# Kernel optimization log

Hardware: AMD Instinct MI355X
Metric: run time of the kernel (lower is better)

Reference implementation:

```python
import jax, jax.numpy as jnp
import numpy as np

B, L, D, H = 2, 4096, 1024, 1  # head_dim == embed_dim in source, forcing H=1


def setup_inputs() -> dict:
    key = jax.random.key(0)
    k_x, kq, kk, kv, ko = jax.random.split(key, 5)
    s = 1.0 / np.sqrt(D)
    return {
        "x": jax.random.normal(k_x, (B, L, D), dtype=jnp.float32),
        "W_q": jax.random.normal(kq, (D, D), dtype=jnp.float32) * s,
        "W_k": jax.random.normal(kk, (D, D), dtype=jnp.float32) * s,
        "W_v": jax.random.normal(kv, (D, D), dtype=jnp.float32) * s,
        "W_o": jax.random.normal(ko, (D, D), dtype=jnp.float32) * s,
    }


def reference(x, W_q, W_k, W_v, W_o):
    # nn.Linear(y) = y @ W.T ; weights stored as (out, in)
    Hd = D  # head_dim = embed_dim (source quirk), so num_heads must be 1
    Q = jnp.einsum('bld,ed->ble', x, W_q).reshape(B, L, H, Hd).transpose(0, 2, 1, 3)
    K = jnp.einsum('bld,ed->ble', x, W_k).reshape(B, L, H, Hd).transpose(0, 2, 1, 3)
    V = jnp.einsum('bld,ed->ble', x, W_v).reshape(B, L, H, Hd).transpose(0, 2, 1, 3)
    scores = jnp.einsum('bhqd,bhkd->bhqk', Q, K) / jnp.sqrt(jnp.float32(Hd))
    attn = jax.nn.softmax(scores, axis=-1)
    out = jnp.einsum('bhqk,bhkd->bhqd', attn, V)  # (B,H,L,Hd)
    out = out.transpose(0, 2, 1, 3).reshape(B, L, D)
    return jnp.einsum('bld,ed->ble', out, W_o)
```

## Files before the change

### kernel.cpp

```cpp
#include <hip/hip_runtime.h>
#include <hip/hip_bf16.h>
#include <stdint.h>


typedef unsigned short u16;
typedef short short8 __attribute__((ext_vector_type(8)));
typedef float f32x4 __attribute__((ext_vector_type(4)));

__device__ __forceinline__ void async_ld16(void* lds, const void* g) {
  __builtin_amdgcn_global_load_lds(
      (const __attribute__((address_space(1))) unsigned int*)g,
      (__attribute__((address_space(3))) unsigned int*)lds,
      16, 0, 0);
}

__device__ __forceinline__ u16 f2bf(float f) {
  unsigned u = __float_as_uint(f);
  u += 0x7FFFu + ((u >> 16) & 1u);
  return (u16)(u >> 16);
}

__global__ __launch_bounds__(256)
void cast_f32_bf16(const float* __restrict__ in, u16* __restrict__ out, int n) {
  const int i = (blockIdx.x * 256 + threadIdx.x) * 8;
  if (i >= n) return;
  float4 a = ((const float4*)(in + i))[0];
  float4 b = ((const float4*)(in + i))[1];
  uint4 o;
  o.x = (unsigned)f2bf(a.x) | ((unsigned)f2bf(a.y) << 16);
  o.y = (unsigned)f2bf(a.z) | ((unsigned)f2bf(a.w) << 16);
  o.z = (unsigned)f2bf(b.x) | ((unsigned)f2bf(b.y) << 16);
  o.w = (unsigned)f2bf(b.z) | ((unsigned)f2bf(b.w) << 16);
  *(uint4*)(out + i) = o;
}

__global__ __launch_bounds__(256)
void cast_w4_bf16(const float* __restrict__ w0, const float* __restrict__ w1,
                  const float* __restrict__ w2, const float* __restrict__ w3,
                  u16* __restrict__ out) {
  const int idx = (blockIdx.x * 256 + threadIdx.x) * 8;
  const int which = idx >> 20;
  const int off = idx & 1048575;
  const float* src = which == 0 ? w0 : which == 1 ? w1 : which == 2 ? w2 : w3;
  float4 a = ((const float4*)(src + off))[0];
  float4 b = ((const float4*)(src + off))[1];
  uint4 o;
  o.x = (unsigned)f2bf(a.x) | ((unsigned)f2bf(a.y) << 16);
  o.y = (unsigned)f2bf(a.z) | ((unsigned)f2bf(a.w) << 16);
  o.z = (unsigned)f2bf(b.x) | ((unsigned)f2bf(b.y) << 16);
  o.w = (unsigned)f2bf(b.z) | ((unsigned)f2bf(b.w) << 16);
  *(uint4*)(out + idx) = o;
}

#define BM 128
#define BN 128
#define BK 32

template <int XSWZ>
__global__ __launch_bounds__(256)
void gemm_bt(const u16* __restrict__ A, const u16* __restrict__ Bt,
             void* __restrict__ Cv, int K, int lda, int ldb, int ldc,
             long long sAz, long long sBz, long long sCz,
             float scale, int store_f32) {
  __shared__ u16 As[3][BM * BK];
  __shared__ u16 Bs[3][BN * BK];

  int bx, by, bz;
  if constexpr (XSWZ) {
    const int gx = gridDim.x, gy = gridDim.y;
    const int nwg = gx * gy * gridDim.z;
    const int lin = (blockIdx.z * gy + blockIdx.y) * gx + blockIdx.x;
    const int chunk = nwg >> 3;
    const int swz = (lin & 7) * chunk + (lin >> 3);
    bx = swz % gx;
    const int t1 = swz / gx;
    by = t1 % gy;
    bz = t1 / gy;
  } else {
    bx = blockIdx.x; by = blockIdx.y; bz = blockIdx.z;
  }

  A  += (long long)bz * sAz;
  Bt += (long long)bz * sBz;

  const int tid  = threadIdx.x;
  const int wave = tid >> 6;
  const int lane = tid & 63;
  const int wm   = wave >> 1;
  const int wn   = wave & 1;
  const int r15  = lane & 15;
  const int q4   = lane >> 4;

  const int tileM = by * BM;
  const int tileN = bx * BN;

  const int srow = tid >> 2;
  const int scol = ((tid & 3) ^ (srow & 3)) * 8;

  const u16* Aptr = A + (long long)tileM * lda + scol;
  const u16* Bptr = Bt + (long long)tileN * ldb + scol;

  auto stage = [&](int kt) {
    const int b = kt % 3;
    const int k0 = kt * BK;
    u16* as = &As[b][tid * 8];
    u16* bs = &Bs[b][tid * 8];
    async_ld16(as,        Aptr + (long long)srow * lda + k0);
    async_ld16(as + 2048, Aptr + (long long)(srow + 64) * lda + k0);
    async_ld16(bs,        Bptr + (long long)srow * ldb + k0);
    async_ld16(bs + 2048, Bptr + (long long)(srow + 64) * ldb + k0);
  };

  f32x4 zero = {0.f, 0.f, 0.f, 0.f};
  f32x4 acc[4][4];
#pragma unroll
  for (int i = 0; i < 4; ++i)
#pragma unroll
    for (int j = 0; j < 4; ++j) acc[i][j] = zero;

  const int csw = ((q4 ^ (r15 & 3)) * 8);

  const int NT = K / BK;
  stage(0);
  if (NT > 1) stage(1);
  if (NT > 2) stage(2);

  for (int kt = 0; kt < NT; ++kt) {
    const int rem = NT - 1 - kt;
    if (rem >= 2)      asm volatile("s_waitcnt vmcnt(8)" ::: "memory");
    else if (rem == 1) asm volatile("s_waitcnt vmcnt(4)" ::: "memory");
    else               asm volatile("s_waitcnt vmcnt(0)" ::: "memory");
    __builtin_amdgcn_s_barrier();

    const int b = kt % 3;
    const u16* as = &As[b][0];
    const u16* bs = &Bs[b][0];

    short8 af[4], bf[4];
#pragma unroll
    for (int i = 0; i < 4; ++i)
      af[i] = *(const short8*)&as[(wm * 64 + i * 16 + r15) * BK + csw];
#pragma unroll
    for (int i = 0; i < 4; ++i)
      bf[i] = *(const short8*)&bs[(wn * 64 + i * 16 + r15) * BK + csw];

    __builtin_amdgcn_s_setprio(1);
#pragma unroll
    for (int i = 0; i < 4; ++i)
#pragma unroll
      for (int j = 0; j < 4; ++j)
        acc[i][j] = __builtin_amdgcn_mfma_f32_16x16x32_bf16(af[i], bf[j], acc[i][j], 0, 0, 0);
    __builtin_amdgcn_s_setprio(0);

    __builtin_amdgcn_s_barrier();
    if (kt + 3 < NT) stage(kt + 3);
  }

#pragma unroll
  for (int i = 0; i < 4; ++i) {
#pragma unroll
    for (int j = 0; j < 4; ++j) {
      const int col = tileN + wn * 64 + j * 16 + r15;
#pragma unroll
      for (int r = 0; r < 4; ++r) {
        const int row = tileM + wm * 64 + i * 16 + q4 * 4 + r;
        const long long idx = (long long)bz * sCz + (long long)row * ldc + col;
        const float val = acc[i][j][r] * scale;
        if (store_f32) ((float*)Cv)[idx] = val;
        else           ((u16*)Cv)[idx] = f2bf(val);
      }
    }
  }
}

__global__ __launch_bounds__(256)
void softmax_rows(u16* __restrict__ S) {
  const int tid = threadIdx.x;
  u16* rp = S + (long long)blockIdx.x * 4096;

  uint4 a = ((const uint4*)rp)[tid * 2];
  uint4 b = ((const uint4*)rp)[tid * 2 + 1];
  unsigned w[8] = {a.x, a.y, a.z, a.w, b.x, b.y, b.z, b.w};
  float v[16];
#pragma unroll
  for (int i = 0; i < 8; ++i) {
    v[2 * i]     = __uint_as_float(w[i] << 16);
    v[2 * i + 1] = __uint_as_float(w[i] & 0xFFFF0000u);
  }

  float m = v[0];
#pragma unroll
  for (int i = 1; i < 16; ++i) m = fmaxf(m, v[i]);
#pragma unroll
  for (int o = 32; o > 0; o >>= 1) m = fmaxf(m, __shfl_xor(m, o));
  __shared__ float redm[4];
  __shared__ float reds[4];
  const int wave = tid >> 6;
  if ((tid & 63) == 0) redm[wave] = m;
  __syncthreads();
  m = fmaxf(fmaxf(redm[0], redm[1]), fmaxf(redm[2], redm[3]));

  float s = 0.f;
#pragma unroll
  for (int i = 0; i < 16; ++i) {
    v[i] = __expf(v[i] - m);
    s += v[i];
  }
#pragma unroll
  for (int o = 32; o > 0; o >>= 1) s += __shfl_xor(s, o);
  if ((tid & 63) == 0) reds[wave] = s;
  __syncthreads();
  s = (reds[0] + reds[1]) + (reds[2] + reds[3]);
  const float inv = 1.0f / s;

#pragma unroll
  for (int i = 0; i < 8; ++i)
    w[i] = (unsigned)f2bf(v[2 * i] * inv) | ((unsigned)f2bf(v[2 * i + 1] * inv) << 16);
  uint4 oa = {w[0], w[1], w[2], w[3]};
  uint4 ob = {w[4], w[5], w[6], w[7]};
  ((uint4*)rp)[tid * 2] = oa;
  ((uint4*)rp)[tid * 2 + 1] = ob;
}

extern "C" void kernel_launch(void* const* d_in, const int* in_sizes, int n_in,
                              void* d_out, int out_size, void* d_ws, size_t ws_size,
                              hipStream_t stream) {
  const float* x  = (const float*)d_in[0];
  const float* Wq = (const float*)d_in[1];
  const float* Wk = (const float*)d_in[2];
  const float* Wv = (const float*)d_in[3];
  const float* Wo = (const float*)d_in[4];
  float* out = (float*)d_out;

  u16* xb  = (u16*)d_ws;
  u16* Wqb = xb  + 8388608;
  u16* Wkb = Wqb + 1048576;
  u16* Wvb = Wkb + 1048576;
  u16* Wob = Wvb + 1048576;
  u16* QKp = Wob + 1048576;
  u16* Vt  = QKp + 16777216;
  u16* S   = Vt  + 8388608;
  u16* O   = QKp;

  const dim3 blk(256);

  cast_f32_bf16<<<dim3(4096), blk, 0, stream>>>(x, xb, 8388608);
  cast_w4_bf16<<<dim3(2048), blk, 0, stream>>>(Wq, Wk, Wv, Wo, Wqb);

  gemm_bt<1><<<dim3(16, 64, 1), blk, 0, stream>>>(xb, Wqb, QKp,
                                                  1024, 1024, 1024, 2048,
                                                  0, 0, 0, 1.f, 0);
  gemm_bt<0><<<dim3(64, 8, 1), blk, 0, stream>>>(Wvb, xb, Vt,
                                                 1024, 1024, 1024, 8192,
                                                 0, 0, 0, 1.f, 0);
  gemm_bt<1><<<dim3(32, 32, 2), blk, 0, stream>>>(QKp, QKp + 1024, S,
                                                  1024, 2048, 2048, 4096,
                                                  8388608LL, 8388608LL, 16777216LL,
                                                  0.03125f, 0);
  softmax_rows<<<dim3(8192), blk, 0, stream>>>(S);
  gemm_bt<1><<<dim3(8, 32, 2), blk, 0, stream>>>(S, Vt, O,
                                                 4096, 4096, 8192, 1024,
                                                 16777216LL, 4096LL, 4194304LL,
                                                 1.f, 0);
  gemm_bt<1><<<dim3(8, 64, 1), blk, 0, stream>>>(O, Wob, out,
                                                 1024, 1024, 1024, 1024,
                                                 0, 0, 0, 1.f, 1);
}
```

Measured before the change: 396.9 us.

## Use 256x256-tile 8-wave pipelined GEMM for QK^T scores

```diff
diff --git a/kernel.cpp b/kernel.cpp
--- a/kernel.cpp
+++ b/kernel.cpp
@@ -173,6 +173,123 @@
   }
 }
 
+__global__ __launch_bounds__(512, 2)
+void gemm256_8ph(const u16* __restrict__ A, const u16* __restrict__ Bt,
+                 u16* __restrict__ C, int K, int lda, int ldb, int ldc,
+                 long long sAz, long long sBz, long long sCz, float scale) {
+  __shared__ u16 smem[49152];
+
+  const int gx = gridDim.x, gy = gridDim.y;
+  const int nwg = gx * gy * gridDim.z;
+  const int lin = (blockIdx.z * gy + blockIdx.y) * gx + blockIdx.x;
+  const int chunk = nwg >> 3;
+  const int swz = (lin & 7) * chunk + (lin >> 3);
+  const int bx = swz % gx;
+  const int t1 = swz / gx;
+  const int by = t1 % gy;
+  const int bz = t1 / gy;
+
+  A  += (long long)bz * sAz;
+  Bt += (long long)bz * sBz;
+  const long long cbase = (long long)bz * sCz;
+
+  const int tid  = threadIdx.x;
+  const int wid  = tid >> 6;
+  const int lane = tid & 63;
+  const int wm   = wid >> 2;
+  const int wn   = wid & 3;
+  const int r15  = lane & 15;
+  const int q4   = lane >> 4;
+
+  const int tileM = by * 256;
+  const int tileN = bx * 256;
+
+  const int sr  = tid >> 2;
+  const int gc8 = ((((tid & 3) - ((tid >> 3) & 3)) & 3)) * 8;
+
+  const u16* Asrc = A  + (long long)(tileM + sr) * lda + gc8;
+  const u16* Bsrc = Bt + (long long)(tileN + sr) * ldb + gc8;
+
+  auto stage2A = [&](int kt) {
+    u16* d = &smem[(kt % 3) * 16384 + tid * 8];
+    async_ld16(d,        Asrc + kt * 32);
+    async_ld16(d + 4096, Asrc + (long long)128 * lda + kt * 32);
+  };
+  auto stage2B = [&](int kt) {
+    u16* d = &smem[(kt % 3) * 16384 + 8192 + tid * 8];
+    async_ld16(d,        Bsrc + kt * 32);
+    async_ld16(d + 4096, Bsrc + (long long)128 * ldb + kt * 32);
+  };
+
+  const int csw = (((q4 + (r15 >> 1)) & 3)) * 8;
+
+  f32x4 acc[8][4];
+#pragma unroll
+  for (int i = 0; i < 8; ++i)
+#pragma unroll
+    for (int j = 0; j < 4; ++j) acc[i][j] = (f32x4){0.f, 0.f, 0.f, 0.f};
+
+  const int NT = K >> 5;
+
+  stage2A(0); stage2B(0);
+  if (NT > 1) { stage2A(1); stage2B(1); }
+
+  for (int t = 0; t < NT; ++t) {
+    if (t + 1 < NT) asm volatile("s_waitcnt vmcnt(4)" ::: "memory");
+    else            asm volatile("s_waitcnt vmcnt(0)" ::: "memory");
+    __builtin_amdgcn_s_barrier();
+
+    const u16* bufA = &smem[(t % 3) * 16384];
+    const u16* bufB = bufA + 8192;
+
+    short8 bf[4], af[4];
+#pragma unroll
+    for (int j = 0; j < 4; ++j)
+      bf[j] = *(const short8*)&bufB[(wn * 64 + j * 16 + r15) * 32 + csw];
+#pragma unroll
+    for (int i = 0; i < 4; ++i)
+      af[i] = *(const short8*)&bufA[(wm * 128 + i * 16 + r15) * 32 + csw];
+    if (t + 2 < NT) stage2A(t + 2);
+    __builtin_amdgcn_s_barrier();
+
+    __builtin_amdgcn_s_setprio(1);
+#pragma unroll
+    for (int i = 0; i < 4; ++i)
+#pragma unroll
+      for (int j = 0; j < 4; ++j)
+        acc[i][j] = __builtin_amdgcn_mfma_f32_16x16x32_bf16(af[i], bf[j], acc[i][j], 0, 0, 0);
+    __builtin_amdgcn_s_setprio(0);
+    __builtin_amdgcn_s_barrier();
+
+#pragma unroll
+    for (int i = 0; i < 4; ++i)
+      af[i] = *(const short8*)&bufA[(wm * 128 + 64 + i * 16 + r15) * 32 + csw];
+    if (t + 2 < NT) stage2B(t + 2);
+    __builtin_amdgcn_s_barrier();
+
+    __builtin_amdgcn_s_setprio(1);
+#pragma unroll
+    for (int i = 0; i < 4; ++i)
+#pragma unroll
+      for (int j = 0; j < 4; ++j)
+        acc[4 + i][j] = __builtin_amdgcn_mfma_f32_16x16x32_bf16(af[i], bf[j], acc[4 + i][j], 0, 0, 0);
+    __builtin_amdgcn_s_setprio(0);
+    __builtin_amdgcn_s_barrier();
+  }
+
+  const int crow = tileM + wm * 128 + q4 * 4;
+  const int ccol = tileN + wn * 64 + r15;
+#pragma unroll
+  for (int mi = 0; mi < 8; ++mi)
+#pragma unroll
+    for (int nj = 0; nj < 4; ++nj)
+#pragma unroll
+      for (int r = 0; r < 4; ++r) {
+        const long long row = crow + mi * 16 + r;
+        C[cbase + row * ldc + (ccol + nj * 16)] = f2bf(acc[mi][nj][r] * scale);
+      }
+}
+
 __global__ __launch_bounds__(256)
 void softmax_rows(u16* __restrict__ S) {
   const int tid = threadIdx.x;
@@ -253,10 +370,9 @@
   gemm_bt<0><<<dim3(64, 8, 1), blk, 0, stream>>>(Wvb, xb, Vt,
                                                  1024, 1024, 1024, 8192,
                                                  0, 0, 0, 1.f, 0);
-  gemm_bt<1><<<dim3(32, 32, 2), blk, 0, stream>>>(QKp, QKp + 1024, S,
-                                                  1024, 2048, 2048, 4096,
-                                                  8388608LL, 8388608LL, 16777216LL,
-                                                  0.03125f, 0);
+  gemm256_8ph<<<dim3(16, 16, 2), dim3(512), 0, stream>>>(
+      QKp, QKp + 1024, S, 1024, 2048, 2048, 4096,
+      8388608LL, 8388608LL, 16777216LL, 0.03125f);
   softmax_rows<<<dim3(8192), blk, 0, stream>>>(S);
   gemm_bt<1><<<dim3(8, 32, 2), blk, 0, stream>>>(S, Vt, O,
                                                  4096, 4096, 8192, 1024,
```

After: 389.8 us. About the same (-1.8%).
